# Kernel tuning notes

Measured on AMD Instinct MI355X. Metric: run time of the kernel, lower is better.

## Reference

```python
import math
import jax, jax.numpy as jnp
import numpy as np

B, L, DM = 2, 1024, 1024
STATE, EXPAND, CONV, DTR = 16, 2, 4, 8
INNER = DM * EXPAND          # 2048
NFFT = L // 2 + 1            # 513


def _silu(v):
    return v * jax.nn.sigmoid(v)


def setup_inputs() -> dict:
    key = jax.random.key(0)
    ks = jax.random.split(key, 12)
    s = lambda k, shape, sc=0.02: (jax.random.normal(k, shape, jnp.float32) * sc)
    # dt_proj bias initialized like the torch module: exp(U(0,1)*(log dt_max - log dt_min) + log dt_min)
    inv_dt = jnp.exp(jax.random.uniform(ks[10], (INNER,), jnp.float32)
                     * (math.log(0.1) - math.log(0.001)) + math.log(0.001))
    return {
        "x": jax.random.normal(ks[0], (B, L, DM), jnp.float32),
        "in_proj_w": s(ks[1], (2 * INNER, DM)),
        "conv_w": s(ks[2], (INNER, 1, CONV), 0.1),      # depthwise conv kernel
        "conv_b": jnp.zeros((INNER,), jnp.float32),
        "A_log": jnp.tile(jnp.log(jnp.arange(1, STATE + 1, dtype=jnp.float32)), (INNER, 1)),
        "D": jnp.ones((INNER,), jnp.float32),
        "x_proj_w": s(ks[3], (DTR + 2 * STATE, INNER)),
        "dt_proj_w": s(ks[4], (INNER, DTR)),
        "dt_proj_b": inv_dt,
        "filter_real": s(ks[5], (INNER, NFFT)),
        "filter_imag": s(ks[6], (INNER, NFFT)),
        "spectral_decay": jnp.ones((INNER,), jnp.float32) * 0.01,
        "fusion_w": s(ks[7], (INNER, 2 * INNER)),
        "fusion_b": jnp.zeros((INNER,), jnp.float32),
        "out_proj_w": s(ks[8], (DM, INNER)),
        "ln_gamma": jnp.ones((DM,), jnp.float32),
        "ln_beta": jnp.zeros((DM,), jnp.float32),
    }


def reference(x, in_proj_w, conv_w, conv_b, A_log, D, x_proj_w, dt_proj_w, dt_proj_b,
              filter_real, filter_imag, spectral_decay, fusion_w, fusion_b,
              out_proj_w, ln_gamma, ln_beta):
    residual = x
    xz = x @ in_proj_w.T                                   # [B,L,2*INNER]
    x_inner, z = xz[..., :INNER], xz[..., INNER:]
    z = _silu(z)

    # ---- SSM path ----
    xc = jnp.swapaxes(x_inner, 1, 2)                       # [B,E,L]
    xc = jax.lax.conv_general_dilated(
        xc, conv_w, (1,), [(CONV - 1, 0)],                 # causal depthwise conv (pad-left == torch pad + truncate)
        dimension_numbers=("NCH", "OIH", "NCH"),
        feature_group_count=INNER) + conv_b[None, :, None]
    x_conv = jnp.swapaxes(_silu(xc), 1, 2)                 # [B,L,E]

    x_dbc = x_conv @ x_proj_w.T                            # [B,L,DTR+2S]
    dt_x = x_dbc[..., :DTR]
    Bm = x_dbc[..., DTR:DTR + STATE]                       # [B,L,S]
    Cm = x_dbc[..., DTR + STATE:]                          # [B,L,S]
    dt = jax.nn.softplus(dt_x @ dt_proj_w.T + dt_proj_b)   # [B,L,E]
    A = -jnp.exp(A_log)                                    # [E,S]
    dA = jnp.exp(dt[..., None] * A)                        # [B,L,E,S]
    dBx = (dt * x_conv)[..., None] * Bm[:, :, None, :]     # [B,L,E,S]

    def step(h, inp):
        dA_t, dBx_t, C_t = inp
        h = dA_t * h + dBx_t                               # [B,E,S]
        return h, jnp.einsum('bes,bs->be', h, C_t)

    h0 = jnp.zeros((B, INNER, STATE), x.dtype)
    _, ys = jax.lax.scan(step, h0,
                         (jnp.swapaxes(dA, 0, 1), jnp.swapaxes(dBx, 0, 1), jnp.swapaxes(Cm, 0, 1)))
    y_ssm = jnp.swapaxes(ys, 0, 1) + x_conv * D            # [B,L,E]

    # ---- Spectral path ----
    xf = jnp.fft.rfft(jnp.swapaxes(x_inner, 1, 2), axis=-1)        # [B,E,NFFT]
    freqs = jnp.linspace(0.0, 1.0, NFFT)
    filt = (filter_real + 1j * filter_imag) * jnp.exp(-spectral_decay[:, None] * freqs[None, :])
    y_spec = jnp.swapaxes(jnp.fft.irfft(xf * filt[None], n=L, axis=-1), 1, 2)  # [B,L,E]

    # ---- Gated fusion ----
    g = jax.nn.sigmoid(jnp.concatenate([y_ssm, y_spec], -1) @ fusion_w.T + fusion_b)
    y = g * y_ssm + (1.0 - g) * y_spec
    y = y * z
    out = y @ out_proj_w.T + residual                      # [B,L,DM]

    mu = out.mean(-1, keepdims=True)
    var = out.var(-1, keepdims=True)
    return (out - mu) / jnp.sqrt(var + 1e-5) * ln_gamma + ln_beta
```

## Files before the change

### kernel.cpp

```cpp
#include <hip/hip_runtime.h>
#include <math.h>

#define B_ 2
#define L_ 1024
#define DM_ 1024
#define STATE_ 16
#define CONV_ 4
#define DTR_ 8
#define INNER_ 2048
#define M_ (B_*L_)
#define MD_ (B_*INNER_)
#define NFFT_ 513
#define NFP_ 1152
#define NCH_ 32
#define CHL_ 32
#define SK_ 32
#define KSL_ (2048/SK_)

typedef unsigned short u16;
typedef __attribute__((ext_vector_type(8))) short short8;
typedef __attribute__((ext_vector_type(8))) __bf16 bf16x8;
typedef __attribute__((ext_vector_type(4))) float f32x4;

__device__ __forceinline__ float frcp_(float x) { return __builtin_amdgcn_rcpf(x); }
__device__ __forceinline__ float fexp_(float x) { return __expf(x); }
__device__ __forceinline__ float fsigm_(float x) { return frcp_(1.f + __expf(-x)); }
__device__ __forceinline__ float fsilu_(float x) { return x * frcp_(1.f + __expf(-x)); }
__device__ __forceinline__ float fsoftplus_(float v) {
  return (v > 20.f) ? v : __logf(1.f + __expf(v));
}
__device__ __forceinline__ u16 f2bf(float f) {
  union { float f; unsigned u; } v; v.f = f;
  unsigned r = v.u + 0x7fffu + ((v.u >> 16) & 1u);
  return (u16)(r >> 16);
}
__device__ __forceinline__ float bf2f(u16 h) {
  union { unsigned u; float f; } v; v.u = ((unsigned)h) << 16;
  return v.f;
}
__device__ __forceinline__ void gload16(const void* g, void* l) {
  __builtin_amdgcn_global_load_lds(
      (const __attribute__((address_space(1))) unsigned*)g,
      (__attribute__((address_space(3))) unsigned*)l, 16, 0, 0);
}
__device__ __forceinline__ f32x4 mfma_bf16(short8 a, short8 b, f32x4 c) {
  return __builtin_amdgcn_mfma_f32_16x16x32_bf16(
      __builtin_bit_cast(bf16x8, a), __builtin_bit_cast(bf16x8, b), c, 0, 0, 0);
}

#define CVT_N0 2097152
#define CVT_N1 6291456
#define CVT_N2 14680064
#define CVT_NT 16777216
__global__ __launch_bounds__(256) void cvt4_k(
    const float* __restrict__ s0, const float* __restrict__ s1,
    const float* __restrict__ s2, const float* __restrict__ s3,
    u16* __restrict__ out)
{
  int i = (blockIdx.x*256 + threadIdx.x) * 4;
  const float* src; int off;
  if (i < CVT_N0)      { src = s0; off = 0; }
  else if (i < CVT_N1) { src = s1; off = CVT_N0; }
  else if (i < CVT_N2) { src = s2; off = CVT_N1; }
  else                 { src = s3; off = CVT_N2; }
  float4 v = *(const float4*)(src + (i - off));
  ushort4 o;
  o.x = f2bf(v.x); o.y = f2bf(v.y); o.z = f2bf(v.z); o.w = f2bf(v.w);
  *(ushort4*)(out + i) = o;
}

template<int TM, int TN, int EPI>
__global__ __launch_bounds__((TM/64)*(TN/32)*64) void mgemm_k(
    const u16* __restrict__ Ab, const u16* __restrict__ Bb,
    void* __restrict__ Cout, int K, int ldc,
    const float* __restrict__ aux0, u16* __restrict__ aux1,
    const float* __restrict__ aux2, const float* __restrict__ aux3)
{
  constexpr int WN   = TN/32;
  constexpr int NW   = (TM/64)*WN;
  constexpr int NTHR = NW*64;
  __shared__ __align__(16) u16 As[2][TM*64];
  __shared__ __align__(16) u16 Bs[2][TN*64];
  const int t = threadIdx.x;
  const int lane = t & 63;
  const int w = t >> 6;
  const int wm = w / WN, wn = w % WN;
  const int M0 = blockIdx.y * TM, N0 = blockIdx.x * TN;

  f32x4 acc[4][2] = {};

  auto stage = [&](int buf, int k0) {
    #pragma unroll
    for (int q = 0; q < TM*8/NTHR; q++) {
      int u = q*NTHR + t;
      int row = u >> 3, gpr = u & 7;
      int grp = gpr ^ (row & 7);
      gload16(Ab + (size_t)(M0+row)*K + k0 + grp*8, &As[buf][u*8]);
    }
    #pragma unroll
    for (int q = 0; q < TN*8/NTHR; q++) {
      int u = q*NTHR + t;
      int row = u >> 3, gpr = u & 7;
      int grp = gpr ^ (row & 7);
      gload16(Bb + (size_t)(N0+row)*K + k0 + grp*8, &Bs[buf][u*8]);
    }
  };

  stage(0, 0);
  const int nk = K >> 6;
  for (int ks = 0; ks < nk; ks++) {
    const int buf = ks & 1;
    __syncthreads();
    if (ks + 1 < nk) stage(buf ^ 1, (ks + 1) << 6);
    const u16* Asb = As[buf];
    const u16* Bsb = Bs[buf];
    #pragma unroll
    for (int kk = 0; kk < 2; kk++) {
      const int quad = lane >> 4;
      const int grp = kk*4 + quad;
      short8 af[4], bf[2];
      #pragma unroll
      for (int i = 0; i < 4; i++) {
        int row = wm*64 + i*16 + (lane & 15);
        af[i] = *(const short8*)&Asb[(row*8 + (grp ^ (row & 7)))*8];
      }
      #pragma unroll
      for (int j = 0; j < 2; j++) {
        int row = wn*32 + j*16 + (lane & 15);
        bf[j] = *(const short8*)&Bsb[(row*8 + (grp ^ (row & 7)))*8];
      }
      #pragma unroll
      for (int i = 0; i < 4; i++)
        #pragma unroll
        for (int j = 0; j < 2; j++)
          acc[i][j] = mfma_bf16(af[i], bf[j], acc[i][j]);
    }
  }

  #pragma unroll
  for (int i = 0; i < 4; i++) {
    int mbase = M0 + wm*64 + i*16 + (lane >> 4)*4;
    #pragma unroll
    for (int j = 0; j < 2; j++) {
      int n = N0 + wn*32 + j*16 + (lane & 15);
      #pragma unroll
      for (int r = 0; r < 4; r++) {
        int m = mbase + r;
        float v = acc[i][j][r];
        if (EPI == 0) {
          ((float*)Cout)[(size_t)m*ldc + n] = v;
        } else if (EPI == 1) {
          float g  = fsigm_(v + aux0[n]);
          float ys = bf2f(aux1[(size_t)m*4096 + n]);
          float yp = bf2f(aux1[(size_t)m*4096 + 2048 + n]);
          float z  = aux2[(size_t)m*4096 + 2048 + n];
          ((u16*)Cout)[(size_t)m*ldc + n] = f2bf((g*ys + (1.f-g)*yp)*fsilu_(z));
        } else if (EPI == 2) {
          ((float*)Cout)[(size_t)m*ldc + n] = v + aux2[(size_t)m*ldc + n];
        } else if (EPI == 3) {
          float pv = __shfl_xor(v, 1, 64);
          int f = n >> 1;
          float outv = 0.f;
          if (f < NFFT_) {
            int c = m & (INNER_-1);
            float d  = fexp_(-aux2[c] * (float)f * (1.f/512.f));
            float wr = aux0[c*NFFT_+f]*d, wi = aux3[c*NFFT_+f]*d;
            float a = (n & 1) ? pv : v;
            float b = (n & 1) ? v : pv;
            outv = (n & 1) ? (a*wi + b*wr) : (a*wr - b*wi);
          }
          ((u16*)Cout)[(size_t)m*ldc + n] = f2bf(outv);
        } else if (EPI == 5) {
          ((float*)Cout)[(size_t)m*ldc + n] = v;
          if (n < 2048) {
            int b2 = m >> 10, l2 = m & 1023;
            aux1[((size_t)(b2*2048 + n) << 10) + l2] = f2bf(v);
          }
        } else {
          int b2 = m >> 11, c2 = m & (INNER_-1);
          ((u16*)Cout)[((size_t)((b2 << 10) + n) << 12) + 2048 + c2] = f2bf(v);
        }
      }
    }
  }
}

__global__ __launch_bounds__(256) void xproj_k(
    const float* __restrict__ xconv, const float* __restrict__ W,
    float* __restrict__ part)
{
  __shared__ float Bs[40][KSL_+4];
  const int sk = blockIdx.x, mt = blockIdx.y;
  const int k0 = sk*KSL_;
  for (int i = threadIdx.x; i < 40*KSL_; i += 256) {
    int n = i >> 6, k = i & (KSL_-1);
    Bs[n][k] = W[(size_t)n*2048 + k0 + k];
  }
  __syncthreads();
  const int m = mt*256 + threadIdx.x;
  const float* arow = xconv + (size_t)m*2048 + k0;
  float acc[40];
  #pragma unroll
  for (int j=0;j<40;j++) acc[j]=0.f;
  for (int k = 0; k < KSL_; k += 4) {
    float4 a = *(const float4*)(arow + k);
    #pragma unroll
    for (int j = 0; j < 40; j++) {
      float4 b = *(const float4*)&Bs[j][k];
      acc[j] += a.x*b.x + a.y*b.y + a.z*b.z + a.w*b.w;
    }
  }
  float* o = part + ((size_t)sk*M_ + m)*40;
  #pragma unroll
  for (int j = 0; j < 10; j++)
    *(float4*)(o + j*4) = make_float4(acc[j*4], acc[j*4+1], acc[j*4+2], acc[j*4+3]);
}

__global__ __launch_bounds__(256) void xpred_k(const float* __restrict__ part,
                                               float* __restrict__ xdbc)
{
  int i = blockIdx.x*256 + threadIdx.x;
  float s = 0.f;
  #pragma unroll
  for (int sk = 0; sk < SK_; sk++) s += part[(size_t)sk*81920 + i];
  xdbc[i] = s;
}

__global__ __launch_bounds__(256) void conv_silu_k(
    const float* __restrict__ xz, const float* __restrict__ cw,
    const float* __restrict__ cb, float* __restrict__ xc)
{
  int idx = blockIdx.x*256 + threadIdx.x;
  int c = idx & (INNER_-1);
  int g = idx >> 11;
  int b = g >> 7;
  int lb = (g & 127) * 8;
  float w0=cw[c*4+0], w1=cw[c*4+1], w2=cw[c*4+2], w3=cw[c*4+3];
  float bias = cb[c];
  float v[11];
  #pragma unroll
  for (int j = 0; j < 11; j++) {
    int l = lb - 3 + j;
    v[j] = (l >= 0) ? xz[((size_t)((b << 10) + l))*4096 + c] : 0.f;
  }
  #pragma unroll
  for (int j = 0; j < 8; j++) {
    float s = bias + w0*v[j] + w1*v[j+1] + w2*v[j+2] + w3*v[j+3];
    xc[((size_t)((b << 10) + lb + j))*INNER_ + c] = fsilu_(s);
  }
}

__global__ __launch_bounds__(256) void scan1_k(
    const float* __restrict__ xdbc, const float* __restrict__ xconv,
    const float* __restrict__ A_log, const float* __restrict__ dtw,
    const float* __restrict__ dtb, float* __restrict__ Pq)
{
  int idx = blockIdx.x*256 + threadIdx.x;
  int e  = idx & (INNER_-1);
  int bc = idx >> 11;
  int ch = bc & (NCH_-1);
  int b  = bc >> 5;
  float A[STATE_];
  #pragma unroll
  for (int s=0;s<STATE_;s++) A[s] = -fexp_(A_log[e*STATE_+s]);
  float w[DTR_];
  #pragma unroll
  for (int r=0;r<DTR_;r++) w[r] = dtw[e*DTR_+r];
  float bias = dtb[e];
  float h[STATE_] = {};
  float sdt = 0.f;
  int mbase = b*L_ + ch*CHL_;
  float dtx[DTR_], Bv[STATE_], xcv;
  {
    const float* row = xdbc + (size_t)mbase*40;
    #pragma unroll
    for (int r=0;r<DTR_;r++) dtx[r] = row[r];
    #pragma unroll
    for (int s=0;s<STATE_;s++) Bv[s] = row[8+s];
    xcv = xconv[(size_t)mbase*INNER_ + e];
  }
  for (int l=0;l<CHL_;l++) {
    float ndtx[DTR_], nBv[STATE_], nxcv = 0.f;
    if (l+1 < CHL_) {
      const float* nrow = xdbc + (size_t)(mbase+l+1)*40;
      #pragma unroll
      for (int r=0;r<DTR_;r++) ndtx[r] = nrow[r];
      #pragma unroll
      for (int s=0;s<STATE_;s++) nBv[s] = nrow[8+s];
      nxcv = xconv[(size_t)(mbase+l+1)*INNER_ + e];
    } else {
      #pragma unroll
      for (int r=0;r<DTR_;r++) ndtx[r] = 0.f;
      #pragma unroll
      for (int s=0;s<STATE_;s++) nBv[s] = 0.f;
    }
    float v = bias;
    #pragma unroll
    for (int r=0;r<DTR_;r++) v += dtx[r]*w[r];
    float dt = fsoftplus_(v);
    sdt += dt;
    float dx = dt * xcv;
    #pragma unroll
    for (int s=0;s<STATE_;s++) {
      float dA = fexp_(dt*A[s]);
      h[s] = dA*h[s] + dx*Bv[s];
    }
    #pragma unroll
    for (int r=0;r<DTR_;r++) dtx[r] = ndtx[r];
    #pragma unroll
    for (int s=0;s<STATE_;s++) Bv[s] = nBv[s];
    xcv = nxcv;
  }
  float* o = Pq + (size_t)idx*32;
  #pragma unroll
  for (int s=0;s<STATE_;s++) { o[s] = fexp_(A[s]*sdt); o[16+s] = h[s]; }
}

__global__ __launch_bounds__(256) void scan2_k(float* __restrict__ Pq)
{
  int idx = blockIdx.x*256 + threadIdx.x;
  int s = idx & 15;
  int e = (idx >> 4) & (INNER_-1);
  int b = idx >> 15;
  float h = 0.f;
  for (int ch = 0; ch < NCH_; ch++) {
    size_t base = ((size_t)(b*NCH_+ch)*INNER_ + e)*32;
    float p = Pq[base + s];
    float q = Pq[base + 16 + s];
    Pq[base + 16 + s] = h;
    h = p*h + q;
  }
}

__global__ __launch_bounds__(256) void scan3_k(
    const float* __restrict__ xdbc, const float* __restrict__ xconv,
    const float* __restrict__ A_log, const float* __restrict__ dtw,
    const float* __restrict__ dtb, const float* __restrict__ Dp,
    const float* __restrict__ Pq, u16* __restrict__ ycat)
{
  int idx = blockIdx.x*256 + threadIdx.x;
  int e  = idx & (INNER_-1);
  int bc = idx >> 11;
  int ch = bc & (NCH_-1);
  int b  = bc >> 5;
  float A[STATE_];
  #pragma unroll
  for (int s=0;s<STATE_;s++) A[s] = -fexp_(A_log[e*STATE_+s]);
  float w[DTR_];
  #pragma unroll
  for (int r=0;r<DTR_;r++) w[r] = dtw[e*DTR_+r];
  float bias = dtb[e];
  float Dv = Dp[e];
  float h[STATE_];
  const float* hi = Pq + (size_t)idx*32 + 16;
  #pragma unroll
  for (int s=0;s<STATE_;s++) h[s] = hi[s];
  int mbase = b*L_ + ch*CHL_;
  float dtx[DTR_], Bv[STATE_], Cv[STATE_], xcv;
  {
    const float* row = xdbc + (size_t)mbase*40;
    #pragma unroll
    for (int r=0;r<DTR_;r++) dtx[r] = row[r];
    #pragma unroll
    for (int s=0;s<STATE_;s++) { Bv[s] = row[8+s]; Cv[s] = row[24+s]; }
    xcv = xconv[(size_t)mbase*INNER_ + e];
  }
  for (int l=0;l<CHL_;l++) {
    float ndtx[DTR_], nBv[STATE_], nCv[STATE_], nxcv = 0.f;
    if (l+1 < CHL_) {
      const float* nrow = xdbc + (size_t)(mbase+l+1)*40;
      #pragma unroll
      for (int r=0;r<DTR_;r++) ndtx[r] = nrow[r];
      #pragma unroll
      for (int s=0;s<STATE_;s++) { nBv[s] = nrow[8+s]; nCv[s] = nrow[24+s]; }
      nxcv = xconv[(size_t)(mbase+l+1)*INNER_ + e];
    } else {
      #pragma unroll
      for (int r=0;r<DTR_;r++) ndtx[r] = 0.f;
      #pragma unroll
      for (int s=0;s<STATE_;s++) { nBv[s] = 0.f; nCv[s] = 0.f; }
    }
    float v = bias;
    #pragma unroll
    for (int r=0;r<DTR_;r++) v += dtx[r]*w[r];
    float dt = fsoftplus_(v);
    float dx = dt * xcv;
    float y = 0.f;
    #pragma unroll
    for (int s=0;s<STATE_;s++) {
      float dA = fexp_(dt*A[s]);
      h[s] = dA*h[s] + dx*Bv[s];
      y += h[s]*Cv[s];
    }
    ycat[(size_t)(mbase+l)*4096 + e] = f2bf(y + xcv*Dv);
    #pragma unroll
    for (int r=0;r<DTR_;r++) dtx[r] = ndtx[r];
    #pragma unroll
    for (int s=0;s<STATE_;s++) { Bv[s] = nBv[s]; Cv[s] = nCv[s]; }
    xcv = nxcv;
  }
}

__global__ __launch_bounds__(256) void genWdftb_k(u16* __restrict__ W) {
  int idx = blockIdx.x*256 + threadIdx.x;
  int l = idx & (L_-1);
  int col = idx >> 10;
  float v = 0.f;
  int f = col >> 1;
  if (f < NFFT_) {
    int ph = (l*f) & (L_-1);
    float th = (float)ph * (6.283185307179586f / (float)L_);
    v = (col & 1) ? -__sinf(th) : __cosf(th);
  }
  W[idx] = f2bf(v);
}

__global__ __launch_bounds__(256) void genWinvb_k(u16* __restrict__ W) {
  int idx = blockIdx.x*256 + threadIdx.x;
  int r = idx % NFP_;
  int l = idx / NFP_;
  int f = r >> 1;
  float v = 0.f;
  if (f < NFFT_) {
    bool edge = (f == 0) || (f == 512);
    float sc = (edge ? 1.f : 2.f) / (float)L_;
    int ph = (f*l) & (L_-1);
    float th = (float)ph * (6.283185307179586f / (float)L_);
    if (r & 1) v = edge ? 0.f : -sc*__sinf(th);
    else       v = sc*__cosf(th);
  }
  W[idx] = f2bf(v);
}

__global__ __launch_bounds__(256) void ln_k(const float* __restrict__ inp,
    const float* __restrict__ gma, const float* __restrict__ bta,
    float* __restrict__ out)
{
  int m = blockIdx.x;
  const float* row = inp + (size_t)m*DM_;
  float s=0.f, s2=0.f;
  float v[4];
  #pragma unroll
  for (int j=0;j<4;j++) {
    v[j] = row[threadIdx.x + j*256];
    s += v[j]; s2 += v[j]*v[j];
  }
  #pragma unroll
  for (int off=32; off>=1; off>>=1) {
    s  += __shfl_down(s, off);
    s2 += __shfl_down(s2, off);
  }
  __shared__ float rs[4], rs2[4], stats[2];
  int wid = threadIdx.x >> 6;
  if ((threadIdx.x & 63) == 0) { rs[wid]=s; rs2[wid]=s2; }
  __syncthreads();
  if (threadIdx.x == 0) {
    float ts  = rs[0]+rs[1]+rs[2]+rs[3];
    float ts2 = rs2[0]+rs2[1]+rs2[2]+rs2[3];
    float mu  = ts/(float)DM_;
    float var = ts2/(float)DM_ - mu*mu;
    stats[0] = mu; stats[1] = rsqrtf(var + 1e-5f);
  }
  __syncthreads();
  float mu = stats[0], rstd = stats[1];
  #pragma unroll
  for (int j=0;j<4;j++) {
    int n = threadIdx.x + j*256;
    out[(size_t)m*DM_ + n] = (v[j]-mu)*rstd*gma[n] + bta[n];
  }
}

extern "C" void kernel_launch(void* const* d_in, const int* in_sizes, int n_in,
                              void* d_out, int out_size, void* d_ws, size_t ws_size,
                              hipStream_t stream)
{
  const float* x       = (const float*)d_in[0];
  const float* in_w    = (const float*)d_in[1];
  const float* conv_w  = (const float*)d_in[2];
  const float* conv_b  = (const float*)d_in[3];
  const float* A_log   = (const float*)d_in[4];
  const float* Dp      = (const float*)d_in[5];
  const float* xproj_w = (const float*)d_in[6];
  const float* dt_w    = (const float*)d_in[7];
  const float* dt_b    = (const float*)d_in[8];
  const float* f_re    = (const float*)d_in[9];
  const float* f_im    = (const float*)d_in[10];
  const float* s_dec   = (const float*)d_in[11];
  const float* fus_w   = (const float*)d_in[12];
  const float* fus_b   = (const float*)d_in[13];
  const float* out_w   = (const float*)d_in[14];
  const float* ln_g    = (const float*)d_in[15];
  const float* ln_b    = (const float*)d_in[16];
  float* out = (float*)d_out;

  float* ws    = (float*)d_ws;
  float* xz    = ws;
  float* xconv = xz    + 8388608;
  float* xdbc  = xconv + 4194304;
  float* Pq    = xdbc  + 81920;
  u16* ub      = (u16*)(Pq + 4194304);
  u16* xb      = ub;
  u16* inwb    = xb    + 2097152;
  u16* fuswb   = inwb  + 4194304;
  u16* outwb   = fuswb + 8388608;
  u16* xt      = outwb + 2097152;
  u16* Wb      = xt    + 4194304;
  u16* XFb     = Wb    + 1179648;
  u16* ycat    = XFb   + 4718592;
  u16* ycomb   = xt;
  float* outp  = xconv;
  float* part  = (float*)ycat;

  cvt4_k<<<CVT_NT/1024, 256, 0, stream>>>(x, in_w, fus_w, out_w, xb);

  mgemm_k<128,128,5><<<dim3(4096/128, M_/128), 512, 0, stream>>>(
      xb, inwb, xz, 1024, 4096, nullptr, xt, nullptr, nullptr);
  conv_silu_k<<<(M_*INNER_/8)/256, 256, 0, stream>>>(xz, conv_w, conv_b, xconv);
  xproj_k<<<dim3(SK_, M_/256), 256, 0, stream>>>(xconv, xproj_w, part);
  xpred_k<<<(M_*40)/256, 256, 0, stream>>>(part, xdbc);
  scan1_k<<<(B_*NCH_*INNER_)/256, 256, 0, stream>>>(xdbc, xconv, A_log, dt_w, dt_b, Pq);
  scan2_k<<<(B_*INNER_*STATE_)/256, 256, 0, stream>>>(Pq);
  scan3_k<<<(B_*NCH_*INNER_)/256, 256, 0, stream>>>(xdbc, xconv, A_log, dt_w, dt_b, Dp, Pq, ycat);
  genWdftb_k<<<(NFP_*1024)/256, 256, 0, stream>>>(Wb);
  mgemm_k<128,64,3><<<dim3(NFP_/64, MD_/128), 256, 0, stream>>>(
      xt, Wb, XFb, 1024, NFP_, f_re, nullptr, s_dec, f_im);
  genWinvb_k<<<(NFP_*1024)/256, 256, 0, stream>>>(Wb);
  mgemm_k<128,64,6><<<dim3(1024/64, MD_/128), 256, 0, stream>>>(
      XFb, Wb, ycat, NFP_, 0, nullptr, nullptr, nullptr, nullptr);
  mgemm_k<128,64,1><<<dim3(2048/64, M_/128), 256, 0, stream>>>(
      ycat, fuswb, ycomb, 4096, 2048, fus_b, ycat, xz, nullptr);
  mgemm_k<64,64,2><<<dim3(1024/64, M_/64), 128, 0, stream>>>(
      ycomb, outwb, outp, 2048, 1024, nullptr, nullptr, x, nullptr);
  ln_k<<<M_, 256, 0, stream>>>(outp, ln_g, ln_b, out);
}
```

Measured before the change: 410.5 us.

## Split-K fusion and output GEMMs, finer scan chunks, smaller in_proj tiles

```diff
diff --git a/kernel.cpp b/kernel.cpp
--- a/kernel.cpp
+++ b/kernel.cpp
@@ -12,8 +12,8 @@
 #define MD_ (B_*INNER_)
 #define NFFT_ 513
 #define NFP_ 1152
-#define NCH_ 32
-#define CHL_ 32
+#define NCH_ 64
+#define CHL_ 16
 #define SK_ 32
 #define KSL_ (2048/SK_)
 
@@ -72,7 +72,7 @@
 template<int TM, int TN, int EPI>
 __global__ __launch_bounds__((TM/64)*(TN/32)*64) void mgemm_k(
     const u16* __restrict__ Ab, const u16* __restrict__ Bb,
-    void* __restrict__ Cout, int K, int ldc,
+    void* __restrict__ Cout, int klen, int lda, int ldc, int psz,
     const float* __restrict__ aux0, u16* __restrict__ aux1,
     const float* __restrict__ aux2, const float* __restrict__ aux3)
 {
@@ -86,6 +86,7 @@
   const int w = t >> 6;
   const int wm = w / WN, wn = w % WN;
   const int M0 = blockIdx.y * TM, N0 = blockIdx.x * TN;
+  const int kbeg = blockIdx.z * klen;
 
   f32x4 acc[4][2] = {};
 
@@ -95,23 +96,23 @@
       int u = q*NTHR + t;
       int row = u >> 3, gpr = u & 7;
       int grp = gpr ^ (row & 7);
-      gload16(Ab + (size_t)(M0+row)*K + k0 + grp*8, &As[buf][u*8]);
+      gload16(Ab + (size_t)(M0+row)*lda + k0 + grp*8, &As[buf][u*8]);
     }
     #pragma unroll
     for (int q = 0; q < TN*8/NTHR; q++) {
       int u = q*NTHR + t;
       int row = u >> 3, gpr = u & 7;
       int grp = gpr ^ (row & 7);
-      gload16(Bb + (size_t)(N0+row)*K + k0 + grp*8, &Bs[buf][u*8]);
+      gload16(Bb + (size_t)(N0+row)*lda + k0 + grp*8, &Bs[buf][u*8]);
     }
   };
 
-  stage(0, 0);
-  const int nk = K >> 6;
+  stage(0, kbeg);
+  const int nk = klen >> 6;
   for (int ks = 0; ks < nk; ks++) {
     const int buf = ks & 1;
     __syncthreads();
-    if (ks + 1 < nk) stage(buf ^ 1, (ks + 1) << 6);
+    if (ks + 1 < nk) stage(buf ^ 1, kbeg + ((ks + 1) << 6));
     const u16* Asb = As[buf];
     const u16* Bsb = Bs[buf];
     #pragma unroll
@@ -148,15 +149,7 @@
         int m = mbase + r;
         float v = acc[i][j][r];
         if (EPI == 0) {
-          ((float*)Cout)[(size_t)m*ldc + n] = v;
-        } else if (EPI == 1) {
-          float g  = fsigm_(v + aux0[n]);
-          float ys = bf2f(aux1[(size_t)m*4096 + n]);
-          float yp = bf2f(aux1[(size_t)m*4096 + 2048 + n]);
-          float z  = aux2[(size_t)m*4096 + 2048 + n];
-          ((u16*)Cout)[(size_t)m*ldc + n] = f2bf((g*ys + (1.f-g)*yp)*fsilu_(z));
-        } else if (EPI == 2) {
-          ((float*)Cout)[(size_t)m*ldc + n] = v + aux2[(size_t)m*ldc + n];
+          ((float*)Cout)[(size_t)blockIdx.z*psz + (size_t)m*ldc + n] = v;
         } else if (EPI == 3) {
           float pv = __shfl_xor(v, 1, 64);
           int f = n >> 1;
@@ -185,6 +178,75 @@
   }
 }
 
+__global__ __launch_bounds__(256) void fcomb_k(
+    const float* __restrict__ pF, const float* __restrict__ fb,
+    const u16* __restrict__ ycat, const float* __restrict__ xz,
+    u16* __restrict__ ycomb)
+{
+  int idx = blockIdx.x*256 + threadIdx.x;
+  int m = idx >> 9;
+  int n = (idx & 511) * 4;
+  float4 a = *(const float4*)(pF + (size_t)m*2048 + n);
+  float4 b = *(const float4*)(pF + 4194304 + (size_t)m*2048 + n);
+  float4 fbv = *(const float4*)(fb + n);
+  ushort4 ysu = *(const ushort4*)(ycat + (size_t)m*4096 + n);
+  ushort4 ypu = *(const ushort4*)(ycat + (size_t)m*4096 + 2048 + n);
+  float4 zv = *(const float4*)(xz + (size_t)m*4096 + 2048 + n);
+  float pre[4] = {a.x+b.x+fbv.x, a.y+b.y+fbv.y, a.z+b.z+fbv.z, a.w+b.w+fbv.w};
+  float ys[4] = {bf2f(ysu.x), bf2f(ysu.y), bf2f(ysu.z), bf2f(ysu.w)};
+  float yp[4] = {bf2f(ypu.x), bf2f(ypu.y), bf2f(ypu.z), bf2f(ypu.w)};
+  float z[4] = {zv.x, zv.y, zv.z, zv.w};
+  ushort4 o;
+  u16* op = (u16*)&o;
+  #pragma unroll
+  for (int j = 0; j < 4; j++) {
+    float g = fsigm_(pre[j]);
+    op[j] = f2bf((g*ys[j] + (1.f-g)*yp[j]) * fsilu_(z[j]));
+  }
+  *(ushort4*)(ycomb + (size_t)m*2048 + n) = o;
+}
+
+__global__ __launch_bounds__(256) void oln_k(
+    const float* __restrict__ pO, const float* __restrict__ x,
+    const float* __restrict__ gma, const float* __restrict__ bta,
+    float* __restrict__ out)
+{
+  int m = blockIdx.x;
+  float s=0.f, s2=0.f;
+  float v[4];
+  #pragma unroll
+  for (int j=0;j<4;j++) {
+    int n = threadIdx.x + j*256;
+    size_t p = (size_t)m*DM_ + n;
+    float val = pO[p] + pO[2097152 + p] + x[p];
+    v[j] = val;
+    s += val; s2 += val*val;
+  }
+  #pragma unroll
+  for (int off=32; off>=1; off>>=1) {
+    s  += __shfl_down(s, off);
+    s2 += __shfl_down(s2, off);
+  }
+  __shared__ float rs[4], rs2[4], stats[2];
+  int wid = threadIdx.x >> 6;
+  if ((threadIdx.x & 63) == 0) { rs[wid]=s; rs2[wid]=s2; }
+  __syncthreads();
+  if (threadIdx.x == 0) {
+    float ts  = rs[0]+rs[1]+rs[2]+rs[3];
+    float ts2 = rs2[0]+rs2[1]+rs2[2]+rs2[3];
+    float mu  = ts/(float)DM_;
+    float var = ts2/(float)DM_ - mu*mu;
+    stats[0] = mu; stats[1] = rsqrtf(var + 1e-5f);
+  }
+  __syncthreads();
+  float mu = stats[0], rstd = stats[1];
+  #pragma unroll
+  for (int j=0;j<4;j++) {
+    int n = threadIdx.x + j*256;
+    out[(size_t)m*DM_ + n] = (v[j]-mu)*rstd*gma[n] + bta[n];
+  }
+}
+
 __global__ __launch_bounds__(256) void xproj_k(
     const float* __restrict__ xconv, const float* __restrict__ W,
     float* __restrict__ part)
@@ -253,13 +315,14 @@
 __global__ __launch_bounds__(256) void scan1_k(
     const float* __restrict__ xdbc, const float* __restrict__ xconv,
     const float* __restrict__ A_log, const float* __restrict__ dtw,
-    const float* __restrict__ dtb, float* __restrict__ Pq)
+    const float* __restrict__ dtb, float* __restrict__ qbuf,
+    float* __restrict__ sdtb)
 {
   int idx = blockIdx.x*256 + threadIdx.x;
   int e  = idx & (INNER_-1);
   int bc = idx >> 11;
   int ch = bc & (NCH_-1);
-  int b  = bc >> 5;
+  int b  = bc >> 6;
   float A[STATE_];
   #pragma unroll
   for (int s=0;s<STATE_;s++) A[s] = -fexp_(A_log[e*STATE_+s]);
@@ -311,23 +374,27 @@
     for (int s=0;s<STATE_;s++) Bv[s] = nBv[s];
     xcv = nxcv;
   }
-  float* o = Pq + (size_t)idx*32;
-  #pragma unroll
-  for (int s=0;s<STATE_;s++) { o[s] = fexp_(A[s]*sdt); o[16+s] = h[s]; }
-}
-
-__global__ __launch_bounds__(256) void scan2_k(float* __restrict__ Pq)
+  sdtb[idx] = sdt;
+  float* o = qbuf + (size_t)idx*16;
+  #pragma unroll
+  for (int s=0;s<STATE_;s++) o[s] = h[s];
+}
+
+__global__ __launch_bounds__(256) void scan2_k(float* __restrict__ qbuf,
+                                               const float* __restrict__ sdtb,
+                                               const float* __restrict__ A_log)
 {
   int idx = blockIdx.x*256 + threadIdx.x;
   int s = idx & 15;
   int e = (idx >> 4) & (INNER_-1);
   int b = idx >> 15;
+  float As = -fexp_(A_log[e*STATE_+s]);
   float h = 0.f;
   for (int ch = 0; ch < NCH_; ch++) {
-    size_t base = ((size_t)(b*NCH_+ch)*INNER_ + e)*32;
-    float p = Pq[base + s];
-    float q = Pq[base + 16 + s];
-    Pq[base + 16 + s] = h;
+    size_t tix = ((size_t)(b*NCH_+ch)*INNER_ + e);
+    float p = fexp_(As * sdtb[tix]);
+    float q = qbuf[tix*16 + s];
+    qbuf[tix*16 + s] = h;
     h = p*h + q;
   }
 }
@@ -336,13 +403,13 @@
     const float* __restrict__ xdbc, const float* __restrict__ xconv,
     const float* __restrict__ A_log, const float* __restrict__ dtw,
     const float* __restrict__ dtb, const float* __restrict__ Dp,
-    const float* __restrict__ Pq, u16* __restrict__ ycat)
+    const float* __restrict__ qbuf, u16* __restrict__ ycat)
 {
   int idx = blockIdx.x*256 + threadIdx.x;
   int e  = idx & (INNER_-1);
   int bc = idx >> 11;
   int ch = bc & (NCH_-1);
-  int b  = bc >> 5;
+  int b  = bc >> 6;
   float A[STATE_];
   #pragma unroll
   for (int s=0;s<STATE_;s++) A[s] = -fexp_(A_log[e*STATE_+s]);
@@ -352,7 +419,7 @@
   float bias = dtb[e];
   float Dv = Dp[e];
   float h[STATE_];
-  const float* hi = Pq + (size_t)idx*32 + 16;
+  const float* hi = qbuf + (size_t)idx*16;
   #pragma unroll
   for (int s=0;s<STATE_;s++) h[s] = hi[s];
   int mbase = b*L_ + ch*CHL_;
@@ -430,44 +497,6 @@
     else       v = sc*__cosf(th);
   }
   W[idx] = f2bf(v);
-}
-
-__global__ __launch_bounds__(256) void ln_k(const float* __restrict__ inp,
-    const float* __restrict__ gma, const float* __restrict__ bta,
-    float* __restrict__ out)
-{
-  int m = blockIdx.x;
-  const float* row = inp + (size_t)m*DM_;
-  float s=0.f, s2=0.f;
-  float v[4];
-  #pragma unroll
-  for (int j=0;j<4;j++) {
-    v[j] = row[threadIdx.x + j*256];
-    s += v[j]; s2 += v[j]*v[j];
-  }
-  #pragma unroll
-  for (int off=32; off>=1; off>>=1) {
-    s  += __shfl_down(s, off);
-    s2 += __shfl_down(s2, off);
-  }
-  __shared__ float rs[4], rs2[4], stats[2];
-  int wid = threadIdx.x >> 6;
-  if ((threadIdx.x & 63) == 0) { rs[wid]=s; rs2[wid]=s2; }
-  __syncthreads();
-  if (threadIdx.x == 0) {
-    float ts  = rs[0]+rs[1]+rs[2]+rs[3];
-    float ts2 = rs2[0]+rs2[1]+rs2[2]+rs2[3];
-    float mu  = ts/(float)DM_;
-    float var = ts2/(float)DM_ - mu*mu;
-    stats[0] = mu; stats[1] = rsqrtf(var + 1e-5f);
-  }
-  __syncthreads();
-  float mu = stats[0], rstd = stats[1];
-  #pragma unroll
-  for (int j=0;j<4;j++) {
-    int n = threadIdx.x + j*256;
-    out[(size_t)m*DM_ + n] = (v[j]-mu)*rstd*gma[n] + bta[n];
-  }
 }
 
 extern "C" void kernel_launch(void* const* d_in, const int* in_sizes, int n_in,
@@ -495,10 +524,10 @@
 
   float* ws    = (float*)d_ws;
   float* xz    = ws;
-  float* xconv = xz    + 8388608;
-  float* xdbc  = xconv + 4194304;
-  float* Pq    = xdbc  + 81920;
-  u16* ub      = (u16*)(Pq + 4194304);
+  float* xdbc  = xz    + 8388608;
+  float* xconv = xdbc  + 81920;
+  float* qbuf  = xconv + 4194304;
+  u16* ub      = (u16*)(qbuf + 4194304);
   u16* xb      = ub;
   u16* inwb    = xb    + 2097152;
   u16* fuswb   = inwb  + 4194304;
@@ -508,28 +537,31 @@
   u16* XFb     = Wb    + 1179648;
   u16* ycat    = XFb   + 4718592;
   u16* ycomb   = xt;
-  float* outp  = xconv;
+  float* sdtb  = (float*)Wb;
   float* part  = (float*)ycat;
+  float* partF = xconv;
+  float* partO = xconv;
 
   cvt4_k<<<CVT_NT/1024, 256, 0, stream>>>(x, in_w, fus_w, out_w, xb);
 
-  mgemm_k<128,128,5><<<dim3(4096/128, M_/128), 512, 0, stream>>>(
-      xb, inwb, xz, 1024, 4096, nullptr, xt, nullptr, nullptr);
+  mgemm_k<128,64,5><<<dim3(4096/64, M_/128), 256, 0, stream>>>(
+      xb, inwb, xz, 1024, 1024, 4096, 0, nullptr, xt, nullptr, nullptr);
   conv_silu_k<<<(M_*INNER_/8)/256, 256, 0, stream>>>(xz, conv_w, conv_b, xconv);
   xproj_k<<<dim3(SK_, M_/256), 256, 0, stream>>>(xconv, xproj_w, part);
   xpred_k<<<(M_*40)/256, 256, 0, stream>>>(part, xdbc);
-  scan1_k<<<(B_*NCH_*INNER_)/256, 256, 0, stream>>>(xdbc, xconv, A_log, dt_w, dt_b, Pq);
-  scan2_k<<<(B_*INNER_*STATE_)/256, 256, 0, stream>>>(Pq);
-  scan3_k<<<(B_*NCH_*INNER_)/256, 256, 0, stream>>>(xdbc, xconv, A_log, dt_w, dt_b, Dp, Pq, ycat);
+  scan1_k<<<(B_*NCH_*INNER_)/256, 256, 0, stream>>>(xdbc, xconv, A_log, dt_w, dt_b, qbuf, sdtb);
+  scan2_k<<<(B_*INNER_*STATE_)/256, 256, 0, stream>>>(qbuf, sdtb, A_log);
+  scan3_k<<<(B_*NCH_*INNER_)/256, 256, 0, stream>>>(xdbc, xconv, A_log, dt_w, dt_b, Dp, qbuf, ycat);
   genWdftb_k<<<(NFP_*1024)/256, 256, 0, stream>>>(Wb);
   mgemm_k<128,64,3><<<dim3(NFP_/64, MD_/128), 256, 0, stream>>>(
-      xt, Wb, XFb, 1024, NFP_, f_re, nullptr, s_dec, f_im);
+      xt, Wb, XFb, 1024, 1024, NFP_, 0, f_re, nullptr, s_dec, f_im);
   genWinvb_k<<<(NFP_*1024)/256, 256, 0, stream>>>(Wb);
   mgemm_k<128,64,6><<<dim3(1024/64, MD_/128), 256, 0, stream>>>(
-      XFb, Wb, ycat, NFP_, 0, nullptr, nullptr, nullptr, nullptr);
-  mgemm_k<128,64,1><<<dim3(2048/64, M_/128), 256, 0, stream>>>(
-      ycat, fuswb, ycomb, 4096, 2048, fus_b, ycat, xz, nullptr);
-  mgemm_k<64,64,2><<<dim3(1024/64, M_/64), 128, 0, stream>>>(
-      ycomb, outwb, outp, 2048, 1024, nullptr, nullptr, x, nullptr);
-  ln_k<<<M_, 256, 0, stream>>>(outp, ln_g, ln_b, out);
-}
+      XFb, Wb, ycat, NFP_, NFP_, 0, 0, nullptr, nullptr, nullptr, nullptr);
+  mgemm_k<128,64,0><<<dim3(2048/64, M_/128, 2), 256, 0, stream>>>(
+      ycat, fuswb, partF, 2048, 4096, 2048, 4194304, nullptr, nullptr, nullptr, nullptr);
+  fcomb_k<<<(M_*2048/4)/256, 256, 0, stream>>>(partF, fus_b, ycat, xz, ycomb);
+  mgemm_k<128,64,0><<<dim3(1024/64, M_/128, 2), 256, 0, stream>>>(
+      ycomb, outwb, partO, 1024, 2048, 1024, 2097152, nullptr, nullptr, nullptr, nullptr);
+  oln_k<<<M_, 256, 0, stream>>>(partO, x, ln_g, ln_b, out);
+}
```

Result: slower. 419.3 us (+2.1%).
